# Kernel tuning notes

Measured on AMD Instinct MI355X. Metric: run time of the kernel, lower is better.

The kernel has to match this reference:

```python
import jax, jax.numpy as jnp
import numpy as np
from jax import lax

N = 4096
E = 131072
C = 128
CH = [(128, 256), (256, 512), (512, 512), (512, 256), (256, 128)]


def setup_inputs() -> dict:
    key = jax.random.key(0)
    ks = jax.random.split(key, 16)
    inp = {}
    inp["x"] = jax.random.normal(ks[0], (N, C), jnp.float32)
    src = jax.random.randint(ks[1], (E,), 0, N)
    dst = jax.random.randint(ks[2], (E,), 0, N)
    inp["edge_index"] = jnp.stack([src, dst]).astype(jnp.int32)
    for i, (ci, co) in enumerate(CH):
        inp[f"theta{i}"] = jax.random.normal(ks[3 + i], (ci, co), jnp.float32) / np.float32(np.sqrt(ci))
        inp[f"b{i}"] = jax.random.normal(ks[8 + i], (co,), jnp.float32) * 0.02
    inp["p1"] = jax.random.normal(ks[13], (256,), jnp.float32)
    inp["p2"] = jax.random.normal(ks[14], (512,), jnp.float32)
    return inp


def gcn(x, W, theta, b):
    """GCNConv with edge weights, dense-adjacency form.
    A_hat = W + I (self loops, weight 1); deg = row-sum of A_hat;
    out[i] = sum_{(r->i)} d^-1/2[r] * w * d^-1/2[i] * (x@theta)[r] + b."""
    n = W.shape[0]
    A = W + jnp.eye(n, dtype=W.dtype)
    deg = A.sum(axis=1)
    dinv = jnp.where(deg > 0, lax.rsqrt(deg), 0.0)
    An = dinv[:, None] * A * dinv[None, :]
    return An.T @ (x @ theta) + b


def augment_adj(W):
    """add_self_loops -> spspmm(A, A) -> remove_self_loops, dense form."""
    n = W.shape[0]
    A = W + jnp.eye(n, dtype=W.dtype)
    A2 = A @ A
    return A2 * (1.0 - jnp.eye(n, dtype=W.dtype))


def topk_pool(x, W, p, k):
    """TopKPooling (ratio fixed via static k, single graph)."""
    score = jnp.tanh((x @ p) / jnp.linalg.norm(p))
    vals, perm = lax.top_k(score, k)
    xp = x[perm] * vals[:, None]
    Wp = W[perm][:, perm]  # filter_adj on surviving nodes
    return xp, Wp, perm


def reference(x, edge_index, theta0, theta1, theta2, theta3, theta4,
              b0, b1, b2, b3, b4, p1, p2):
    n = x.shape[0]
    # dense weighted adjacency from edge list (edge_weight = ones, duplicates sum)
    W = jnp.zeros((n, n), x.dtype).at[edge_index[0], edge_index[1]].add(1.0)

    # down block 0
    x0 = jax.nn.relu(gcn(x, W, theta0, b0))                 # [N, 256]
    x1, W1, perm1 = topk_pool(x0, augment_adj(W), p1, n // 2)
    # down block 1
    x1b = jax.nn.relu(gcn(x1, W1, theta1, b1))              # [N/2, 512]
    x2, W2, perm2 = topk_pool(x1b, augment_adj(W1), p2, n // 4)
    # bottleneck block
    xb = jax.nn.relu(gcn(x2, W2, theta2, b2))               # [N/4, 512]
    summary = xb.mean(axis=0, keepdims=True)                # global_mean_pool, 1 graph
    # up block (i=3): edges[1]=W1, res=x1b, perm2
    up1 = jnp.zeros_like(x1b).at[perm2].set(xb)
    xu = jax.nn.relu(gcn(x1b + up1, W1, theta3, b3))        # [N/2, 256]
    # up block (i=4): edges[0]=W, res=x0, perm1
    up0 = jnp.zeros_like(x0).at[perm1].set(xu)
    xout = jax.nn.relu(gcn(x0 + up0, W, theta4, b4))        # [N, 128]
    return xout, summary
```

## Files before the change

kernel.cpp:

```cpp
#include <hip/hip_runtime.h>

#define N0 4096
#define P1K 2048
#define P2K 1024
#define SPLITS 4

typedef short bf16x8 __attribute__((ext_vector_type(8)));
typedef float f32x4 __attribute__((ext_vector_type(4)));

__device__ __forceinline__ unsigned short f2bf(float f) {
  unsigned int u = __float_as_uint(f);
  unsigned int r = (u + 0x7fff + ((u >> 16) & 1)) >> 16;
  return (unsigned short)r;
}
__device__ __forceinline__ float bf2f(unsigned short h) {
  unsigned int u = ((unsigned int)h) << 16;
  return __uint_as_float(u);
}

__device__ __forceinline__ float blockReduceSum256(float v) {
  __shared__ float sh[16];
  int lane = threadIdx.x & 63;
  int w = threadIdx.x >> 6;
#pragma unroll
// ... 66 lines not shown
    o0h[(size_t)n * 128 + k] = h;
    o0l[(size_t)n * 128 + k] = f2bf(v - bf2f(h));
  } else if (idx < 163840) {
    int i = idx - 32768;
    int k = i >> 9, n = i & 511;
    float v = t1[i];
    unsigned short h = f2bf(v);
    o1h[(size_t)n * 256 + k] = h;
    o1l[(size_t)n * 256 + k] = f2bf(v - bf2f(h));
  } else if (idx < 425984) {
    int i = idx - 163840;
    int k = i >> 9, n = i & 511;
    o2[(size_t)n * 512 + k] = f2bf(t2[i]);
  } else if (idx < 557056) {
    int i = idx - 425984;
    int k = i >> 8, n = i & 255;
    o3[(size_t)n * 512 + k] = f2bf(t3[i]);
  } else if (idx < 589824) {
    int i = idx - 557056;
    int k = i >> 7, n = i & 127;
    o4[(size_t)n * 256 + k] = f2bf(t4[i]);
  }
}

__global__ __launch_bounds__(256) void fused_ce_conv(
    const int* __restrict__ src, const int* __restrict__ dst, int* __restrict__ co,
    int* __restrict__ ci, int E, const float* t0, const float* t1, const float* t2,
    const float* t3, const float* t4, unsigned short* o0h, unsigned short* o0l,
    unsigned short* o1h, unsigned short* o1l, unsigned short* o2, unsigned short* o3,
    unsigned short* o4) {
  if (blockIdx.x < 512) count_edges_body(blockIdx.x, src, dst, co, ci, E);
  else conv_body(blockIdx.x - 512, t0, t1, t2, t3, t4, o0h, o0l, o1h, o1l, o2, o3, o4);
}

__global__ __launch_bounds__(1024) void exscan_dual(const int* __restrict__ co,
                                                    const int* __restrict__ ci,
                                                    int* __restrict__ optr,
                                                    int* __restrict__ iptr,
                                                    float* __restrict__ dinv0) {
  __shared__ int ls[1024];
  const int* cnt = blockIdx.x ? ci : co;
  int* ptr = blockIdx.x ? iptr : optr;
  int t = threadIdx.x;
  int v0 = cnt[t * 4], v1 = cnt[t * 4 + 1], v2 = cnt[t * 4 + 2], v3 = cnt[t * 4 + 3];
  int s = v0 + v1 + v2 + v3;
  ls[t] = s;
  __syncthreads();
  for (int off = 1; off < 1024; off <<= 1) {
    int x = (t >= off) ? ls[t - off] : 0;
    __syncthreads();
    ls[t] += x;
    __syncthreads();
  }
  int ex = (t > 0) ? ls[t - 1] : 0;
  ptr[t * 4]     = ex;
  ptr[t * 4 + 1] = ex + v0;
  ptr[t * 4 + 2] = ex + v0 + v1;
  ptr[t * 4 + 3] = ex + v0 + v1 + v2;
  if (t == 1023) ptr[4096] = ex + s;
  if (blockIdx.x == 0) {
    dinv0[t * 4]     = rsqrtf((float)v0 + 1.f);
    dinv0[t * 4 + 1] = rsqrtf((float)v1 + 1.f);
    dinv0[t * 4 + 2] = rsqrtf((float)v2 + 1.f);
    dinv0[t * 4 + 3] = rsqrtf((float)v3 + 1.f);
  }
}

__device__ __forceinline__ void fill_body(int b, const int* __restrict__ src,
                                          const int* __restrict__ dst,
                                          const int* __restrict__ optr,
                                          const int* __restrict__ iptr,
                                          int* __restrict__ fo, int* __restrict__ fi,
                                          int* __restrict__ odst, int* __restrict__ isrc,
                                          int E) {
  int e = b * 256 + threadIdx.x;
  if (e < E) {
    int s = src[e], d = dst[e];
    odst[optr[s] + atomicAdd(&fo[s], 1)] = d;
    isrc[iptr[d] + atomicAdd(&fi[d], 1)] = s;
  }
}

template <bool TOUT>
__device__ void gemm3_body(int bid, const float* __restrict__ A,
                           const unsigned short* __restrict__ BhT,
                           const unsigned short* __restrict__ BlT,
                           const int* __restrict__ permA, const float* __restrict__ valsA,
                           const float* __restrict__ dinv, float* __restrict__ C,
                           unsigned short* __restrict__ ChT, unsigned short* __restrict__ ClT,
                           int M, int N, int K, int nbx) {
  __shared__ unsigned short U[16384];
  unsigned short* Ah = U;
  unsigned short* Al = U + 4096;
  unsigned short* Bh = U + 8192;
  unsigned short* Bl = U + 12288;
  int tid = threadIdx.x;
  int by = bid / nbx, bx = bid % nbx;
  int row0 = by << 6, col0 = bx << 6;
  int l = tid & 63, wv = tid >> 6;
  int wr = (wv >> 1) << 5, wc = (wv & 1) << 5;
  f32x4 acc[2][2] = {};
  for (int k0 = 0; k0 < K; k0 += 64) {
#pragma unroll
    for (int it = 0; it < 2; ++it) {
      int idx = (it << 8) + tid;
      int r = idx >> 3, c8 = idx & 7;
      int sw = c8 ^ (r & 7);
      int row = row0 + r;
      int srow = permA ? permA[row] : row;
      float vs = valsA ? valsA[row] : 1.f;
      const float* Af = A + (size_t)srow * K + k0 + (c8 << 3);
      float4 f0 = *(const float4*)Af;
      float4 f1 = *(const float4*)(Af + 4);
      float vv[8] = {f0.x * vs, f0.y * vs, f0.z * vs, f0.w * vs,
                     f1.x * vs, f1.y * vs, f1.z * vs, f1.w * vs};
      uint4 uh, ul;
      unsigned short hh[8], ll[8];
#pragma unroll
      for (int q = 0; q < 8; ++q) {
        hh[q] = f2bf(vv[q]);
        ll[q] = f2bf(vv[q] - bf2f(hh[q]));
      }
      uh.x = (unsigned)hh[0] | ((unsigned)hh[1] << 16);
      uh.y = (unsigned)hh[2] | ((unsigned)hh[3] << 16);
      uh.z = (unsigned)hh[4] | ((unsigned)hh[5] << 16);
      uh.w = (unsigned)hh[6] | ((unsigned)hh[7] << 16);
      ul.x = (unsigned)ll[0] | ((unsigned)ll[1] << 16);
      ul.y = (unsigned)ll[2] | ((unsigned)ll[3] << 16);
      ul.z = (unsigned)ll[4] | ((unsigned)ll[5] << 16);
      ul.w = (unsigned)ll[6] | ((unsigned)ll[7] << 16);
      ((uint4*)Ah)[(r << 3) + sw] = uh;
      ((uint4*)Al)[(r << 3) + sw] = ul;
      ((uint4*)Bh)[(r << 3) + sw] =
          *(const uint4*)(BhT + (size_t)(col0 + r) * K + k0 + (c8 << 3));
      ((uint4*)Bl)[(r << 3) + sw] =
          *(const uint4*)(BlT + (size_t)(col0 + r) * K + k0 + (c8 << 3));
    }
    __syncthreads();
#pragma unroll
    for (int kk2 = 0; kk2 < 2; ++kk2) {
      int ch = (kk2 << 2) + (l >> 4);
      int ra = wr + (l & 15), rb = ra + 16;
      int ca = wc + (l & 15), cb = ca + 16;
      int oa0 = (ra << 6) + ((ch ^ (ra & 7)) << 3);
      int oa1 = (rb << 6) + ((ch ^ (rb & 7)) << 3);
      int ob0 = (ca << 6) + ((ch ^ (ca & 7)) << 3);
      int ob1 = (cb << 6) + ((ch ^ (cb & 7)) << 3);
      bf16x8 ah0 = *(const bf16x8*)&Ah[oa0], ah1 = *(const bf16x8*)&Ah[oa1];
      bf16x8 al0 = *(const bf16x8*)&Al[oa0], al1 = *(const bf16x8*)&Al[oa1];
      bf16x8 bh0 = *(const bf16x8*)&Bh[ob0], bh1 = *(const bf16x8*)&Bh[ob1];
      bf16x8 bl0 = *(const bf16x8*)&Bl[ob0], bl1 = *(const bf16x8*)&Bl[ob1];
      acc[0][0] = __builtin_amdgcn_mfma_f32_16x16x32_bf16(ah0, bh0, acc[0][0], 0, 0, 0);
      acc[0][1] = __builtin_amdgcn_mfma_f32_16x16x32_bf16(ah0, bh1, acc[0][1], 0, 0, 0);
      acc[1][0] = __builtin_amdgcn_mfma_f32_16x16x32_bf16(ah1, bh0, acc[1][0], 0, 0, 0);
      acc[1][1] = __builtin_amdgcn_mfma_f32_16x16x32_bf16(ah1, bh1, acc[1][1], 0, 0, 0);
      acc[0][0] = __builtin_amdgcn_mfma_f32_16x16x32_bf16(ah0, bl0, acc[0][0], 0, 0, 0);
      acc[0][1] = __builtin_amdgcn_mfma_f32_16x16x32_bf16(ah0, bl1, acc[0][1], 0, 0, 0);
      acc[1][0] = __builtin_amdgcn_mfma_f32_16x16x32_bf16(ah1, bl0, acc[1][0], 0, 0, 0);
      acc[1][1] = __builtin_amdgcn_mfma_f32_16x16x32_bf16(ah1, bl1, acc[1][1], 0, 0, 0);
      acc[0][0] = __builtin_amdgcn_mfma_f32_16x16x32_bf16(al0, bh0, acc[0][0], 0, 0, 0);
      acc[0][1] = __builtin_amdgcn_mfma_f32_16x16x32_bf16(al0, bh1, acc[0][1], 0, 0, 0);
      acc[1][0] = __builtin_amdgcn_mfma_f32_16x16x32_bf16(al1, bh0, acc[1][0], 0, 0, 0);
      acc[1][1] = __builtin_amdgcn_mfma_f32_16x16x32_bf16(al1, bh1, acc[1][1], 0, 0, 0);
    }
    __syncthreads();
  }
  int lrow = (l >> 4) << 2, lcol = l & 15;
  float* tf = (float*)U;
#pragma unroll
  for (int i = 0; i < 2; ++i)
#pragma unroll
    for (int j = 0; j < 2; ++j) {
      int lc = wc + (j << 4) + lcol;
      int lr0 = wr + (i << 4) + lrow;
      int c = col0 + lc;
#pragma unroll
      for (int rg = 0; rg < 4; ++rg) {
        int lr = lr0 + rg;
        int r = row0 + lr;
        float dv = dinv ? dinv[r] : 1.f;
        float v = acc[i][j][rg] * dv;
        C[(size_t)r * N + c] = v;
        if (TOUT) tf[lr * 65 + lc] = v;
      }
    }
  if (TOUT) {
    __syncthreads();
    for (int it = 0; it < 16; ++it) {
      int idx = (it << 8) + tid;
      int rr = idx >> 6, cc = idx & 63;
      float v = tf[cc * 65 + rr];
      unsigned short h = f2bf(v);
      size_t o = (size_t)(col0 + rr) * M + row0 + cc;
      ChT[o] = h;
      ClT[o] = f2bf(v - bf2f(h));
    }
  }
}

__global__ __launch_bounds__(256) void fused_fill_g3(
    const int* src, const int* dst, const int* optr, const int* iptr, int* fo, int* fi,
    int* odst, int* isrc, int E, const float* x, const unsigned short* t0hT,
    const unsigned short* t0lT, const float* dinv0, float* SA) {
  if (blockIdx.x < 512) fill_body(blockIdx.x, src, dst, optr, iptr, fo, fi, odst, isrc, E);
  else gemm3_body<false>(blockIdx.x - 512, x, t0hT, t0lT, nullptr, nullptr, dinv0, SA,
                         nullptr, nullptr, 4096, 256, 128, 4);
}

__device__ void transpose_body(int bid, const unsigned short* __restrict__ in,
                               unsigned short* __restrict__ out, int n) {
  __shared__ unsigned short t[64][65];
  int nb = n >> 6;
  int bx = bid % nb, by = bid / nb;
  int r0 = by << 6, c0 = bx << 6;
  for (int it = 0; it < 16; ++it) {
    int idx = (it << 8) + threadIdx.x;
    int r = idx >> 6, c = idx & 63;
    t[r][c] = in[(size_t)(r0 + r) * n + c0 + c];
  }
  __syncthreads();
  for (int it = 0; it < 16; ++it) {
    int idx = (it << 8) + threadIdx.x;
    int r = idx >> 6, c = idx & 63;
    out[(size_t)(c0 + r) * n + r0 + c] = t[c][r];
  }
}

__global__ __launch_bounds__(256) void fused_tr_g3(
    const unsigned short* W1b, unsigned short* W1bT, const float* x0,
    const unsigned short* t1hT, const unsigned short* t1lT, const int* perm1,
    const float* vals1, const float* dinv1, float* SA, unsigned short* ZhT,
    unsigned short* ZlT) {
  if (blockIdx.x < 1024) transpose_body(blockIdx.x, W1b, W1bT, 2048);
  else gemm3_body<true>(blockIdx.x - 1024, x0, t1hT, t1lT, perm1, vals1, dinv1, SA,
                        ZhT, ZlT, 2048, 512, 256, 8);
}

__global__ __launch_bounds__(256) void gemm_skd(const unsigned short* __restrict__ A,
                                                const unsigned short* __restrict__ BhT,
                                                const unsigned short* __restrict__ BlT,
                                                float* __restrict__ Pf,
                                                int M, int N, int K, int nbx, int nb2d) {
  __shared__ unsigned short As[4096], Bh[4096], Bl[4096];
  int tid = threadIdx.x;
  int s = blockIdx.x / nb2d;
  int r2 = blockIdx.x % nb2d;
  int by = r2 / nbx, bx = r2 % nbx;
  int row0 = by << 6, col0 = bx << 6;
  int kc = K / SPLITS;
  int ks = s * kc, ke = ks + kc;
  int l = tid & 63, wv = tid >> 6;
  int wr = (wv >> 1) << 5, wc = (wv & 1) << 5;
  f32x4 acc[2][2] = {};
  for (int k0 = ks; k0 < ke; k0 += 64) {
#pragma unroll
    for (int it = 0; it < 2; ++it) {
      int idx = (it << 8) + tid;
      int r = idx >> 3, c8 = idx & 7;
      int sw = c8 ^ (r & 7);
      ((uint4*)As)[(r << 3) + sw] =
          *(const uint4*)(A + (size_t)(row0 + r) * K + k0 + (c8 << 3));
      ((uint4*)Bh)[(r << 3) + sw] =
          *(const uint4*)(BhT + (size_t)(col0 + r) * K + k0 + (c8 << 3));
      ((uint4*)Bl)[(r << 3) + sw] =
          *(const uint4*)(BlT + (size_t)(col0 + r) * K + k0 + (c8 << 3));
    }
    __syncthreads();
#pragma unroll
    for (int kk2 = 0; kk2 < 2; ++kk2) {
      int ch = (kk2 << 2) + (l >> 4);
      int ra = wr + (l & 15), rb = ra + 16;
      int ca = wc + (l & 15), cb = ca + 16;
      bf16x8 a0 = *(const bf16x8*)&As[(ra << 6) + ((ch ^ (ra & 7)) << 3)];
      bf16x8 a1 = *(const bf16x8*)&As[(rb << 6) + ((ch ^ (rb & 7)) << 3)];
      bf16x8 bh0 = *(const bf16x8*)&Bh[(ca << 6) + ((ch ^ (ca & 7)) << 3)];
      bf16x8 bh1 = *(const bf16x8*)&Bh[(cb << 6) + ((ch ^ (cb & 7)) << 3)];
      bf16x8 bl0 = *(const bf16x8*)&Bl[(ca << 6) + ((ch ^ (ca & 7)) << 3)];
      bf16x8 bl1 = *(const bf16x8*)&Bl[(cb << 6) + ((ch ^ (cb & 7)) << 3)];
      acc[0][0] = __builtin_amdgcn_mfma_f32_16x16x32_bf16(a0, bh0, acc[0][0], 0, 0, 0);
      acc[0][1] = __builtin_amdgcn_mfma_f32_16x16x32_bf16(a0, bh1, acc[0][1], 0, 0, 0);
      acc[1][0] = __builtin_amdgcn_mfma_f32_16x16x32_bf16(a1, bh0, acc[1][0], 0, 0, 0);
      acc[1][1] = __builtin_amdgcn_mfma_f32_16x16x32_bf16(a1, bh1, acc[1][1], 0, 0, 0);
      acc[0][0] = __builtin_amdgcn_mfma_f32_16x16x32_bf16(a0, bl0, acc[0][0], 0, 0, 0);
      acc[0][1] = __builtin_amdgcn_mfma_f32_16x16x32_bf16(a0, bl1, acc[0][1], 0, 0, 0);
      acc[1][0] = __builtin_amdgcn_mfma_f32_16x16x32_bf16(a1, bl0, acc[1][0], 0, 0, 0);
      acc[1][1] = __builtin_amdgcn_mfma_f32_16x16x32_bf16(a1, bl1, acc[1][1], 0, 0, 0);
    }
    __syncthreads();
  }
  int lrow = (l >> 4) << 2, lcol = l & 15;
  float* P = Pf + (size_t)s * M * N;
#pragma unroll
  for (int i = 0; i < 2; ++i)
#pragma unroll
    for (int j = 0; j < 2; ++j) {
      int c = col0 + wc + (j << 4) + lcol;
      int r0 = row0 + wr + (i << 4) + lrow;
#pragma unroll
      for (int rg = 0; rg < 4; ++rg)
        P[(size_t)(r0 + rg) * N + c] = acc[i][j][rg];
    }
}

__global__ __launch_bounds__(256) void gemm_sk(const unsigned short* __restrict__ A,
                                               const unsigned short* __restrict__ BT,
                                               float* __restrict__ Pf,
                                               int M, int N, int K, int nbx, int nb2d) {
  __shared__ unsigned short As[4096];
  __shared__ unsigned short Bs[4096];
  int tid = threadIdx.x;
  int s = blockIdx.x / nb2d;
  int r2 = blockIdx.x % nb2d;
  int by = r2 / nbx, bx = r2 % nbx;
  int row0 = by << 6, col0 = bx << 6;
  int kc = K / SPLITS;
  int ks = s * kc, ke = ks + kc;
  int l = tid & 63, wv = tid >> 6;
  int wr = (wv >> 1) << 5, wc = (wv & 1) << 5;
  f32x4 acc[2][2] = {};
  for (int k0 = ks; k0 < ke; k0 += 64) {
#pragma unroll
    for (int it = 0; it < 2; ++it) {
      int idx = (it << 8) + tid;
      int r = idx >> 3, c8 = idx & 7;
      int sw = c8 ^ (r & 7);
      ((uint4*)As)[(r << 3) + sw] =
          *(const uint4*)(A + (size_t)(row0 + r) * K + k0 + (c8 << 3));
      ((uint4*)Bs)[(r << 3) + sw] =
          *(const uint4*)(BT + (size_t)(col0 + r) * K + k0 + (c8 << 3));
    }
    __syncthreads();
#pragma unroll
    for (int kk2 = 0; kk2 < 2; ++kk2) {
      int ch = (kk2 << 2) + (l >> 4);
      int ra = wr + (l & 15), rb = ra + 16;
      int ca = wc + (l & 15), cb = ca + 16;
      bf16x8 a0 = *(const bf16x8*)&As[(ra << 6) + ((ch ^ (ra & 7)) << 3)];
      bf16x8 a1 = *(const bf16x8*)&As[(rb << 6) + ((ch ^ (rb & 7)) << 3)];
      bf16x8 b0 = *(const bf16x8*)&Bs[(ca << 6) + ((ch ^ (ca & 7)) << 3)];
      bf16x8 b1 = *(const bf16x8*)&Bs[(cb << 6) + ((ch ^ (cb & 7)) << 3)];
      acc[0][0] = __builtin_amdgcn_mfma_f32_16x16x32_bf16(a0, b0, acc[0][0], 0, 0, 0);
      acc[0][1] = __builtin_amdgcn_mfma_f32_16x16x32_bf16(a0, b1, acc[0][1], 0, 0, 0);
      acc[1][0] = __builtin_amdgcn_mfma_f32_16x16x32_bf16(a1, b0, acc[1][0], 0, 0, 0);
      acc[1][1] = __builtin_amdgcn_mfma_f32_16x16x32_bf16(a1, b1, acc[1][1], 0, 0, 0);
    }
    __syncthreads();
  }
  int lrow = (l >> 4) << 2, lcol = l & 15;
  float* P = Pf + (size_t)s * M * N;
#pragma unroll
  for (int i = 0; i < 2; ++i)
#pragma unroll
    for (int j = 0; j < 2; ++j) {
      int c = col0 + wc + (j << 4) + lcol;
      int r0 = row0 + wr + (i << 4) + lrow;
#pragma unroll
      for (int rg = 0; rg < 4; ++rg)
        P[(size_t)(r0 + rg) * N + c] = acc[i][j][rg];
    }
}

__device__ void gemm_e_body(int bid, const float* __restrict__ A,
                            const unsigned short* __restrict__ BT,
                            const int* __restrict__ permA, const float* __restrict__ valsA,
                            const float* __restrict__ dinv, int dm,
                            float* __restrict__ Cf, unsigned short* __restrict__ CbT,
                            int M, int N, int K, int nbx) {
  __shared__ char gsm[16640];
  unsigned short* As = (unsigned short*)gsm;
  unsigned short* Bs = (unsigned short*)(gsm + 8192);
  int tid = threadIdx.x;
  int by = bid / nbx, bx = bid % nbx;
  int row0 = by << 6, col0 = bx << 6;
  int l = tid & 63, wv = tid >> 6;
  int wr = (wv >> 1) << 5, wc = (wv & 1) << 5;
  f32x4 acc[2][2] = {};
  for (int k0 = 0; k0 < K; k0 += 64) {
#pragma unroll
    for (int it = 0; it < 2; ++it) {
      int idx = (it << 8) + tid;
      int r = idx >> 3, c8 = idx & 7;
      int sw = c8 ^ (r & 7);
      int row = row0 + r;
      int srow = permA ? permA[row] : row;
      float vs = valsA ? valsA[row] : 1.f;
      const float* Af = A + (size_t)srow * K + k0 + (c8 << 3);
      float4 f0 = *(const float4*)Af;
      float4 f1 = *(const float4*)(Af + 4);
      uint4 u;
      u.x = (unsigned)f2bf(f0.x * vs) | ((unsigned)f2bf(f0.y * vs) << 16);
      u.y = (unsigned)f2bf(f0.z * vs) | ((unsigned)f2bf(f0.w * vs) << 16);
      u.z = (unsigned)f2bf(f1.x * vs) | ((unsigned)f2bf(f1.y * vs) << 16);
      u.w = (unsigned)f2bf(f1.z * vs) | ((unsigned)f2bf(f1.w * vs) << 16);
      ((uint4*)As)[(r << 3) + sw] = u;
      ((uint4*)Bs)[(r << 3) + sw] =
          *(const uint4*)(BT + (size_t)(col0 + r) * K + k0 + (c8 << 3));
    }
    __syncthreads();
#pragma unroll
    for (int kk2 = 0; kk2 < 2; ++kk2) {
      int ch = (kk2 << 2) + (l >> 4);
      int ra = wr + (l & 15), rb = ra + 16;
      int ca = wc + (l & 15), cb = ca + 16;
      bf16x8 a0 = *(const bf16x8*)&As[(ra << 6) + ((ch ^ (ra & 7)) << 3)];
      bf16x8 a1 = *(const bf16x8*)&As[(rb << 6) + ((ch ^ (rb & 7)) << 3)];
      bf16x8 b0 = *(const bf16x8*)&Bs[(ca << 6) + ((ch ^ (ca & 7)) << 3)];
      bf16x8 b1 = *(const bf16x8*)&Bs[(cb << 6) + ((ch ^ (cb & 7)) << 3)];
      acc[0][0] = __builtin_amdgcn_mfma_f32_16x16x32_bf16(a0, b0, acc[0][0], 0, 0, 0);
      acc[0][1] = __builtin_amdgcn_mfma_f32_16x16x32_bf16(a0, b1, acc[0][1], 0, 0, 0);
      acc[1][0] = __builtin_amdgcn_mfma_f32_16x16x32_bf16(a1, b0, acc[1][0], 0, 0, 0);
      acc[1][1] = __builtin_amdgcn_mfma_f32_16x16x32_bf16(a1, b1, acc[1][1], 0, 0, 0);
    }
    __syncthreads();
  }
  int lrow = (l >> 4) << 2, lcol = l & 15;
  float* tf = (float*)gsm;
#pragma unroll
  for (int i = 0; i < 2; ++i)
#pragma unroll
    for (int j = 0; j < 2; ++j) {
      int lc = wc + (j << 4) + lcol;
      int lr0 = wr + (i << 4) + lrow;
      int c = col0 + lc;
#pragma unroll
      for (int rg = 0; rg < 4; ++rg) {
        int lr = lr0 + rg;
        int r = row0 + lr;
        float dv = (dm == 1) ? dinv[r] : 1.f;
        float v = acc[i][j][rg] * dv;
        Cf[(size_t)r * N + c] = v;
        if (CbT) tf[lr * 65 + lc] = v;
      }
    }
  if (CbT) {
    __syncthreads();
    for (int it = 0; it < 16; ++it) {
      int idx = (it << 8) + tid;
      int rr = idx >> 6, cc = idx & 63;
      CbT[(size_t)(col0 + rr) * M + row0 + cc] = f2bf(tf[cc * 65 + rr]);
    }
  }
}

__global__ __launch_bounds__(256) void gemm_e_k(const float* A, const unsigned short* BT,
                                                const int* permA, const float* valsA,
                                                const float* dinv, int dm, float* Cf,
                                                unsigned short* CbT, int M, int N, int K,
                                                int nbx) {
  gemm_e_body(blockIdx.x, A, BT, permA, valsA, dinv, dm, Cf, CbT, M, N, K, nbx);
}

__device__ void mm_w2_body(int bid, const unsigned short* __restrict__ Wb,
                           const unsigned short* __restrict__ WbT,
                           const int* __restrict__ perm2, float* __restrict__ W2f,
                           float* __restrict__ degsum2) {
  __shared__ unsigned short As[4096];
  __shared__ unsigned short Bs[4096];
  __shared__ int pr[64], pc[64];
  int tid = threadIdx.x;
  int s = bid >> 8;
  int t2d = bid & 255;
  int bx = t2d & 15, by = t2d >> 4;
  int row0 = by << 6, col0 = bx << 6;
  int ks = s * 512, ke = ks + 512;
  if (tid < 64) pr[tid] = perm2[row0 + tid];
  else if (tid < 128) pc[tid - 64] = perm2[col0 + tid - 128 + 64];
  __syncthreads();
  int l = tid & 63, wv = tid >> 6;
  int wr = (wv >> 1) << 5, wc = (wv & 1) << 5;
  f32x4 acc[2][2] = {};
  for (int k0 = ks; k0 < ke; k0 += 64) {
#pragma unroll
    for (int it = 0; it < 2; ++it) {
      int idx = (it << 8) + tid;
      int r = idx >> 3, c8 = idx & 7;
      int sw = c8 ^ (r & 7);
      ((uint4*)As)[(r << 3) + sw] =
          *(const uint4*)(Wb + (size_t)pr[r] * 2048 + k0 + (c8 << 3));
      ((uint4*)Bs)[(r << 3) + sw] =
          *(const uint4*)(WbT + (size_t)pc[r] * 2048 + k0 + (c8 << 3));
    }
    __syncthreads();
    if (tid < 64) {
      int r = tid, d = pr[r] - k0;
      if (d >= 0 && d < 64) {
        int ui = (r << 6) + (((d >> 3) ^ (r & 7)) << 3) + (d & 7);
        As[ui] = f2bf(bf2f(As[ui]) + 1.f);
      }
    } else if (tid < 128) {
      int c = tid - 64, d = pc[c] - k0;
      if (d >= 0 && d < 64) {
        int ui = (c << 6) + (((d >> 3) ^ (c & 7)) << 3) + (d & 7);
        Bs[ui] = f2bf(bf2f(Bs[ui]) + 1.f);
      }
    }
    __syncthreads();
#pragma unroll
    for (int kk2 = 0; kk2 < 2; ++kk2) {
      int ch = (kk2 << 2) + (l >> 4);
      int ra = wr + (l & 15), rb = ra + 16;
      int ca = wc + (l & 15), cb = ca + 16;
      bf16x8 a0 = *(const bf16x8*)&As[(ra << 6) + ((ch ^ (ra & 7)) << 3)];
      bf16x8 a1 = *(const bf16x8*)&As[(rb << 6) + ((ch ^ (rb & 7)) << 3)];
      bf16x8 b0 = *(const bf16x8*)&Bs[(ca << 6) + ((ch ^ (ca & 7)) << 3)];
      bf16x8 b1 = *(const bf16x8*)&Bs[(cb << 6) + ((ch ^ (cb & 7)) << 3)];
      acc[0][0] = __builtin_amdgcn_mfma_f32_16x16x32_bf16(a0, b0, acc[0][0], 0, 0, 0);
      acc[0][1] = __builtin_amdgcn_mfma_f32_16x16x32_bf16(a0, b1, acc[0][1], 0, 0, 0);
      acc[1][0] = __builtin_amdgcn_mfma_f32_16x16x32_bf16(a1, b0, acc[1][0], 0, 0, 0);
      acc[1][1] = __builtin_amdgcn_mfma_f32_16x16x32_bf16(a1, b1, acc[1][1], 0, 0, 0);
    }
    __syncthreads();
  }
  int lrow = (l >> 4) << 2, lcol = l & 15;
#pragma unroll
  for (int i = 0; i < 2; ++i)
#pragma unroll
    for (int j = 0; j < 2; ++j) {
      int c = col0 + wc + (j << 4) + lcol;
      int r0 = row0 + wr + (i << 4) + lrow;
#pragma unroll
      for (int rg = 0; rg < 4; ++rg)
        atomicAdd(&W2f[(size_t)(r0 + rg) * 1024 + c], acc[i][j][rg]);
    }
#pragma unroll
  for (int i = 0; i < 2; ++i)
#pragma unroll
    for (int rg = 0; rg < 4; ++rg) {
      float rs = acc[i][0][rg] + acc[i][1][rg];
#pragma unroll
      for (int o = 1; o < 16; o <<= 1) rs += __shfl_xor(rs, o, 64);
      if ((l & 15) == 0) {
        int r = row0 + wr + (i << 4) + lrow + rg;
        atomicAdd(&degsum2[r], rs);
      }
    }
}

__global__ __launch_bounds__(256) void fused_w2_g2a(
    const unsigned short* Wb, const unsigned short* WbT, const int* perm2, float* W2f,
    float* degsum2, const float* x1b, const unsigned short* t2T, const float* vals2,
    float* SA, unsigned short* SAbT) {
  if (blockIdx.x < 1024) mm_w2_body(blockIdx.x, Wb, WbT, perm2, W2f, degsum2);
  else gemm_e_body(blockIdx.x - 1024, x1b, t2T, perm2, vals2, nullptr, 0, SA, SAbT,
                   1024, 512, 512, 8);
}

__global__ __launch_bounds__(256) void w2T(const float* __restrict__ W2f,
                                           const float* __restrict__ degsum2,
                                           unsigned short* __restrict__ W2Tb,
                                           float* __restrict__ dinv2v) {
  __shared__ float t[64][65];
  __shared__ float ds[64];
  int bx = blockIdx.x & 15, by = blockIdx.x >> 4;
  int r0 = by << 6, c0 = bx << 6;
  if (threadIdx.x < 64) {
    int r = r0 + threadIdx.x;
    float dg = degsum2[r] - W2f[(size_t)r * 1024 + r];
    float dv = rsqrtf(dg + 1.f);
    ds[threadIdx.x] = dv;
    if (bx == 0) dinv2v[r] = dv;
  }
  for (int it = 0; it < 16; ++it) {
    int idx = (it << 8) + threadIdx.x;
    int r = idx >> 6, c = idx & 63;
    float v = W2f[(size_t)(r0 + r) * 1024 + c0 + c];
    if (r0 + r == c0 + c) v = 0.f;
    t[r][c] = v;
  }
  __syncthreads();
  for (int it = 0; it < 16; ++it) {
    int idx = (it << 8) + threadIdx.x;
    int rr = idx >> 6, cc = idx & 63;
    W2Tb[(size_t)(c0 + rr) * 1024 + r0 + cc] = f2bf(t[cc][rr] * ds[cc]);
  }
}

__global__ __launch_bounds__(256) void epi_red1(const float* __restrict__ Pf,
                                                const float* __restrict__ Zadd,
                                                const float* __restrict__ dinv,
                                                const float* __restrict__ bias,
                                                const int* __restrict__ permS,
                                                float* __restrict__ scatterDst,
                                                float* __restrict__ outp, int M, int N,
                                                int zs) {
  int g = blockIdx.x * 256 + threadIdx.x;
  size_t base = (size_t)g * 4;
  size_t MN = (size_t)M * N;
  if (base >= MN) return;
  int r = (int)(base / N), c = (int)(base % N);
  float4 a = *(const float4*)&Pf[base];
#pragma unroll
  for (int s = 1; s < SPLITS; ++s) {
    float4 p = *(const float4*)&Pf[s * MN + base];
    a.x += p.x; a.y += p.y; a.z += p.z; a.w += p.w;
  }
  float4 z = *(const float4*)&Zadd[base];
  float dv = dinv[r];
  float zf = zs ? dv : 1.f;
  float4 bb = *(const float4*)&bias[c];
  float4 o;
  o.x = fmaxf(dv * (a.x + zf * z.x) + bb.x, 0.f);
  o.y = fmaxf(dv * (a.y + zf * z.y) + bb.y, 0.f);
  o.z = fmaxf(dv * (a.z + zf * z.z) + bb.z, 0.f);
  o.w = fmaxf(dv * (a.w + zf * z.w) + bb.w, 0.f);
  if (outp) *(float4*)&outp[base] = o;
  if (permS) {
    float4* d = (float4*)&scatterDst[(size_t)permS[r] * N + c];
    float4 cur = *d;
    cur.x += o.x; cur.y += o.y; cur.z += o.z; cur.w += o.w;
    *d = cur;
  }
}

__global__ __launch_bounds__(256) void epi_red1s(const float* __restrict__ Pf,
                                                 const float* __restrict__ Zadd,
                                                 const float* __restrict__ dinv,
                                                 const float* __restrict__ bias,
                                                 const float* __restrict__ pvec,
                                                 float* __restrict__ sc,
                                                 float* __restrict__ outp) {
  __shared__ float shs[2][2][2];
  int li = threadIdx.x & 127;
  int lr = threadIdx.x >> 7;
  int r = blockIdx.x * 2 + lr;
  size_t base = (size_t)r * 512 + li * 4;
  const size_t MN = (size_t)2048 * 512;
  float4 a = *(const float4*)&Pf[base];
#pragma unroll
  for (int s = 1; s < SPLITS; ++s) {
    float4 p = *(const float4*)&Pf[s * MN + base];
    a.x += p.x; a.y += p.y; a.z += p.z; a.w += p.w;
  }
  float4 z = *(const float4*)&Zadd[base];
  float dv = dinv[r];
  float4 bb = *(const float4*)&bias[li * 4];
  float4 o;
  o.x = fmaxf(dv * (a.x + z.x) + bb.x, 0.f);
  o.y = fmaxf(dv * (a.y + z.y) + bb.y, 0.f);
  o.z = fmaxf(dv * (a.z + z.z) + bb.z, 0.f);
  o.w = fmaxf(dv * (a.w + z.w) + bb.w, 0.f);
  *(float4*)&outp[base] = o;
  float4 pv = *(const float4*)&pvec[li * 4];
  float s1 = pv.x * pv.x + pv.y * pv.y + pv.z * pv.z + pv.w * pv.w;
  float s2 = o.x * pv.x + o.y * pv.y + o.z * pv.z + o.w * pv.w;
#pragma unroll
  for (int t = 32; t > 0; t >>= 1) {
    s1 += __shfl_down(s1, t, 64);
    s2 += __shfl_down(s2, t, 64);
  }
  int wir = (threadIdx.x >> 6) & 1;
  if ((threadIdx.x & 63) == 0) { shs[lr][wir][0] = s1; shs[lr][wir][1] = s2; }
  __syncthreads();
  if ((threadIdx.x & 127) == 0) {
    float S1 = shs[lr][0][0] + shs[lr][1][0];
    float S2 = shs[lr][0][1] + shs[lr][1][1];
    sc[r] = tanhf(S2 / sqrtf(S1));
  }
}

template <int C, bool SCORE>
__global__ __launch_bounds__(256) void gcn_spmm4(const int* __restrict__ iptr,
                                                 const int* __restrict__ isrc,
                                                 const float* __restrict__ Z,
                                                 const float* __restrict__ dinv,
                                                 const float* __restrict__ bias,
                                                 const float* __restrict__ pvec,
                                                 float* __restrict__ sc,
                                                 float* __restrict__ outp) {
  constexpr int L = C / 4;
  int li = threadIdx.x % L;
  int i = blockIdx.x * (256 / L) + threadIdx.x / L;
  float4 acc = *(const float4*)(Z + (size_t)i * C + li * 4);
  int beg = iptr[i], end = iptr[i + 1];
  for (int e = beg; e < end; ++e) {
    float4 z = *(const float4*)(Z + (size_t)isrc[e] * C + li * 4);
    acc.x += z.x; acc.y += z.y; acc.z += z.z; acc.w += z.w;
  }
  float d = dinv[i];
  float4 bb = *(const float4*)(bias + li * 4);
  float4 o;
  o.x = fmaxf(d * acc.x + bb.x, 0.f);
  o.y = fmaxf(d * acc.y + bb.y, 0.f);
  o.z = fmaxf(d * acc.z + bb.z, 0.f);
  o.w = fmaxf(d * acc.w + bb.w, 0.f);
  *(float4*)(outp + (size_t)i * C + li * 4) = o;
  if (SCORE) {
    float4 pv = *(const float4*)(pvec + li * 4);
    float s1 = pv.x * pv.x + pv.y * pv.y + pv.z * pv.z + pv.w * pv.w;
    float s2 = o.x * pv.x + o.y * pv.y + o.z * pv.z + o.w * pv.w;
#pragma unroll
    for (int t = 32; t > 0; t >>= 1) {
      s1 += __shfl_down(s1, t, 64);
      s2 += __shfl_down(s2, t, 64);
    }
    if ((threadIdx.x & 63) == 0) sc[i] = tanhf(s2 / sqrtf(s1));
  }
}

__global__ __launch_bounds__(1024) void topk_select(const float* __restrict__ score,
                                                    int n, int k, int* __restrict__ perm,
                                                    float* __restrict__ vals,
                                                    int* __restrict__ rank) {
  __shared__ unsigned int keys[4096];
  __shared__ int hist[256];
  __shared__ int wsums[16];
  __shared__ unsigned int sh_prefix;
  __shared__ int sh_rem;
  int t = threadIdx.x;
  int m = n >> 10;
  for (int i = t; i < n; i += 1024) {
    unsigned int u = __float_as_uint(score[i]);
    keys[i] = u ^ ((unsigned int)((int)u >> 31) | 0x80000000u);
  }
  if (t == 0) { sh_prefix = 0u; sh_rem = k; }
  __syncthreads();
  for (int round = 0; round < 4; ++round) {
    int shift = 24 - (round << 3);
    if (t < 256) hist[t] = 0;
    __syncthreads();
    unsigned int prefix = sh_prefix;
    unsigned int maskhi = (round == 0) ? 0u : (0xFFFFFFFFu << (shift + 8));
    for (int i = t; i < n; i += 1024) {
      unsigned int kk = keys[i];
      if ((kk & maskhi) == prefix) atomicAdd(&hist[(kk >> shift) & 255], 1);
    }
    __syncthreads();
    if (t == 0) {
      int rem = sh_rem, acc = 0, b = 255;
      for (; b > 0; --b) {
        if (acc + hist[b] >= rem) break;
        acc += hist[b];
      }
      sh_rem = rem - acc;
      sh_prefix = prefix | ((unsigned int)b << shift);
    }
    __syncthreads();
  }
  unsigned int thr = sh_prefix;
  int need = sh_rem;
  int base = t * m;
  int f[4];
  int cnt = 0;
#pragma unroll
  for (int j = 0; j < 4; ++j) {
    f[j] = 0;
    if (j < m) { f[j] = (keys[base + j] == thr) ? 1 : 0; cnt += f[j]; }
  }
  int ex = blockScanExclusive(cnt, wsums);
  int sel[4];
  int scnt = 0;
#pragma unroll
  for (int j = 0; j < 4; ++j) {
    sel[j] = 0;
    if (j < m) {
      unsigned int kk = keys[base + j];
      sel[j] = (kk > thr) || (kk == thr && ex < need);
      ex += f[j];
      scnt += sel[j];
    }
  }
  int pos = blockScanExclusive(scnt, wsums);
#pragma unroll
  for (int j = 0; j < 4; ++j) {
    if (j < m) {
      int i = base + j;
      if (sel[j]) {
        unsigned int kk = keys[i];
        unsigned int u = (kk & 0x80000000u) ? (kk ^ 0x80000000u) : ~kk;
        perm[pos] = i;
        vals[pos] = __uint_as_float(u);
        rank[i] = pos;
        pos++;
      } else {
        rank[i] = -1;
      }
    }
  }
}

__global__ __launch_bounds__(256) void build_W1(const int* __restrict__ optr,
                                                const int* __restrict__ odst,
                                                const int* __restrict__ perm1,
                                                const int* __restrict__ rank1,
                                                unsigned short* __restrict__ W1b,
                                                float* __restrict__ dinv1) {
  __shared__ float row[2048];
  int a = blockIdx.x;
  int pa = perm1[a];
  for (int i = threadIdx.x; i < 2048; i += 256) row[i] = 0.f;
  __syncthreads();
  int kbeg = optr[pa], kend = optr[pa + 1];
  int nk = kend - kbeg + 1;
  int wv = threadIdx.x >> 6, lane = threadIdx.x & 63;
  for (int kidx = wv; kidx < nk; kidx += 4) {
    int k = (kidx == 0) ? pa : odst[kbeg + kidx - 1];
    int jbeg = optr[k], jend = optr[k + 1];
    for (int jj = jbeg - 1 + lane; jj < jend; jj += 64) {
      int j = (jj < jbeg) ? k : odst[jj];
      int rb = rank1[j];
      if (rb >= 0) atomicAdd(&row[rb], 1.0f);
    }
  }
  __syncthreads();
  float ssum = 0.f;
  for (int i = threadIdx.x; i < 2048; i += 256) {
    float v = (i == a) ? 0.f : row[i];
    W1b[(size_t)a * 2048 + i] = f2bf(v);
    ssum += v;
  }
  float t = blockReduceSum256(ssum);
  if (threadIdx.x == 0) dinv1[a] = rsqrtf(t + 1.0f);
}

__device__ void mean_cols_body(int c, const float* __restrict__ X, int R, int C,
                               float* __restrict__ outp) {
  float s = 0.f;
  for (int r = threadIdx.x; r < R; r += 256) s += X[(size_t)r * C + c];
  float t = blockReduceSum256(s);
  if (threadIdx.x == 0) outp[c] = t / (float)R;
}

__global__ __launch_bounds__(256) void fused_mean_up1a(
    const float* xb, float* meanOut, const float* x1b, const unsigned short* t3T,
    const float* dinv1, float* SA, unsigned short* SAbT) {
  if (blockIdx.x < 512) mean_cols_body(blockIdx.x, xb, 1024, 512, meanOut);
  else gemm_e_body(blockIdx.x - 512, x1b, t3T, nullptr, nullptr, dinv1, 1, SA, SAbT,
                   2048, 256, 512, 4);
}

extern "C" void kernel_launch(void* const* d_in, const int* in_sizes, int n_in,
                              void* d_out, int out_size, void* d_ws, size_t ws_size,
                              hipStream_t stream) {
  const float* x      = (const float*)d_in[0];
  const int*   eidx   = (const int*)d_in[1];
  const float* theta0 = (const float*)d_in[2];
  const float* b0     = (const float*)d_in[3];
  const float* theta1 = (const float*)d_in[4];
  const float* b1     = (const float*)d_in[5];
  const float* theta2 = (const float*)d_in[6];
  const float* b2     = (const float*)d_in[7];
  const float* theta3 = (const float*)d_in[8];
  const float* b3     = (const float*)d_in[9];
  const float* theta4 = (const float*)d_in[10];
  const float* b4     = (const float*)d_in[11];
  const float* p1     = (const float*)d_in[12];
  const float* p2     = (const float*)d_in[13];
  const int E = in_sizes[1] / 2;
  const int* src = eidx;
  const int* dst = eidx + E;
  float* out = (float*)d_out;

  char* wsb = (char*)d_ws;
  size_t off = 0;
  auto alloc = [&](size_t bytes) -> void* {
    void* p = wsb + off;
    off = (off + bytes + 255) & ~(size_t)255;
    return p;
  };
  char* zblock = (char*)alloc((size_t)4 * N0 * 4 + P2K * 4 + (size_t)P2K * P2K * 4);
  int* cnt4 = (int*)zblock;
  float* degsum2 = (float*)(zblock + (size_t)4 * N0 * 4);
  float* W2f = (float*)(zblock + (size_t)4 * N0 * 4 + P2K * 4);
  size_t zbytes = (size_t)4 * N0 * 4 + P2K * 4 + (size_t)P2K * P2K * 4;

  int* optr  = (int*)alloc((N0 + 1) * 4);
  int* iptr  = (int*)alloc((N0 + 1) * 4);
  int* odst  = (int*)alloc((size_t)E * 4);
  int* isrc  = (int*)alloc((size_t)E * 4);
  int* perm1 = (int*)alloc(P1K * 4);
  int* rank1 = (int*)alloc(N0 * 4);
  int* perm2 = (int*)alloc(P2K * 4);
  int* rank2 = (int*)alloc(P1K * 4);
  float* dinv0 = (float*)alloc(N0 * 4);
  float* dinv1 = (float*)alloc(P1K * 4);
  float* dinv2v = (float*)alloc(P2K * 4);
  float* vals1 = (float*)alloc(P1K * 4);
  float* vals2 = (float*)alloc(P2K * 4);
  float* score = (float*)alloc(N0 * 4);
  float* x0  = (float*)alloc((size_t)N0 * 256 * 4);
  float* x1b = (float*)alloc((size_t)P1K * 512 * 4);
  float* xb  = (float*)alloc((size_t)P2K * 512 * 4);
  float* SA  = (float*)alloc((size_t)P1K * 512 * 4);
  float* Pf  = (float*)alloc((size_t)SPLITS * 1048576 * 4);
  unsigned short* W1b  = (unsigned short*)alloc((size_t)P1K * P1K * 2);
  unsigned short* W1bT = (unsigned short*)alloc((size_t)P1K * P1K * 2);
  unsigned short* W2Tb = (unsigned short*)alloc((size_t)P2K * P2K * 2);
  unsigned short* SAbT = (unsigned short*)alloc((size_t)524288 * 2);
  unsigned short* ZhT  = (unsigned short*)alloc((size_t)512 * 2048 * 2);
  unsigned short* ZlT  = (unsigned short*)alloc((size_t)512 * 2048 * 2);
  unsigned short* t0hT = (unsigned short*)alloc((size_t)256 * 128 * 2);
  unsigned short* t0lT = (unsigned short*)alloc((size_t)256 * 128 * 2);
  unsigned short* t1hT = (unsigned short*)alloc((size_t)512 * 256 * 2);
  unsigned short* t1lT = (unsigned short*)alloc((size_t)512 * 256 * 2);
  unsigned short* t2T  = (unsigned short*)alloc((size_t)512 * 512 * 2);
  unsigned short* t3T  = (unsigned short*)alloc((size_t)256 * 512 * 2);
  unsigned short* t4T  = (unsigned short*)alloc((size_t)128 * 256 * 2);
  (void)ws_size; (void)n_in; (void)out_size;

  int* co = cnt4;
  int* ci = cnt4 + N0;
  int* fo = cnt4 + 2 * N0;
  int* fi = cnt4 + 3 * N0;

  hipMemsetAsync(zblock, 0, zbytes, stream);
  fused_ce_conv<<<512 + 2304, 256, 0, stream>>>(src, dst, co, ci, E, theta0, theta1,
                                                theta2, theta3, theta4, t0hT, t0lT,
                                                t1hT, t1lT, t2T, t3T, t4T);
  exscan_dual<<<2, 1024, 0, stream>>>(co, ci, optr, iptr, dinv0);
  fused_fill_g3<<<512 + 256, 256, 0, stream>>>(src, dst, optr, iptr, fo, fi, odst, isrc,
                                               E, x, t0hT, t0lT, dinv0, SA);
  gcn_spmm4<256, true><<<1024, 256, 0, stream>>>(iptr, isrc, SA, dinv0, b0, p1, score, x0);

  topk_select<<<1, 1024, 0, stream>>>(score, 4096, 2048, perm1, vals1, rank1);
  build_W1<<<2048, 256, 0, stream>>>(optr, odst, perm1, rank1, W1b, dinv1);
  fused_tr_g3<<<1024 + 256, 256, 0, stream>>>(W1b, W1bT, x0, t1hT, t1lT, perm1, vals1,
                                              dinv1, SA, ZhT, ZlT);

  gemm_skd<<<256 * SPLITS, 256, 0, stream>>>(W1bT, ZhT, ZlT, Pf, 2048, 512, 2048, 8, 256);
  epi_red1s<<<1024, 256, 0, stream>>>(Pf, SA, dinv1, b1, p2, score, x1b);

  topk_select<<<1, 1024, 0, stream>>>(score, 2048, 1024, perm2, vals2, rank2);
  fused_w2_g2a<<<1024 + 128, 256, 0, stream>>>(W1b, W1bT, perm2, W2f, degsum2, x1b, t2T,
                                               vals2, SA, SAbT);
  w2T<<<256, 256, 0, stream>>>(W2f, degsum2, W2Tb, dinv2v);

  gemm_sk<<<128 * SPLITS, 256, 0, stream>>>(W2Tb, SAbT, Pf, 1024, 512, 1024, 8, 128);
  epi_red1<<<1024 * 512 / 1024, 256, 0, stream>>>(Pf, SA, dinv2v, b2, perm2, x1b, xb,
                                                  1024, 512, 1);
  fused_mean_up1a<<<512 + 128, 256, 0, stream>>>(xb, out + 524288, x1b, t3T, dinv1,
                                                 SA, SAbT);

  gemm_sk<<<128 * SPLITS, 256, 0, stream>>>(W1bT, SAbT, Pf, 2048, 256, 2048, 4, 128);
  epi_red1<<<2048 * 256 / 1024, 256, 0, stream>>>(Pf, SA, dinv1, b3, perm1, x0, nullptr,
                                                  2048, 256, 0);

  gemm_e_k<<<128, 256, 0, stream>>>(x0, t4T, nullptr, nullptr, dinv0, 1, SA, nullptr,
                                    4096, 128, 256, 2);
  gcn_spmm4<128, false><<<512, 256, 0, stream>>>(iptr, isrc, SA, dinv0, b4, nullptr,
                                                 nullptr, out);
}
```

Baseline: 310.1 us.

## Fold self-loop term into adjacency diagonal and share LDS across fused branches

The self-loop contribution is now encoded by writing 1 on the diagonal of the bf16 W1/W2 adjacency matrices. Previously it was added separately in the epilogues from an fp32 SA buffer. This removes the SA writes in the feature GEMMs and the Zadd reads in the reduction epilogues, and drops the per-tile diagonal patch in mm_w2. Shared memory in the fused kernels is now one buffer sized for the larger branch instead of separate static arrays, which lowers LDS per block. The risk is that the self-loop term now passes through bf16 operands, and the A² computation depends on the diagonal being exactly 1.

```diff
diff --git a/kernel.cpp b/kernel.cpp
--- a/kernel.cpp
+++ b/kernel.cpp
@@ -172,14 +172,14 @@
 }
 
 template <bool TOUT>
-__device__ void gemm3_body(int bid, const float* __restrict__ A,
+__device__ void gemm3_body(char* smem, int bid, const float* __restrict__ A,
                            const unsigned short* __restrict__ BhT,
                            const unsigned short* __restrict__ BlT,
                            const int* __restrict__ permA, const float* __restrict__ valsA,
                            const float* __restrict__ dinv, float* __restrict__ C,
                            unsigned short* __restrict__ ChT, unsigned short* __restrict__ ClT,
                            int M, int N, int K, int nbx) {
-  __shared__ unsigned short U[16384];
+  unsigned short* U = (unsigned short*)smem;
   unsigned short* Ah = U;
   unsigned short* Al = U + 4096;
   unsigned short* Bh = U + 8192;
@@ -256,7 +256,7 @@
     __syncthreads();
   }
   int lrow = (l >> 4) << 2, lcol = l & 15;
-  float* tf = (float*)U;
+  float* tf = (float*)smem;
 #pragma unroll
   for (int i = 0; i < 2; ++i)
 #pragma unroll
@@ -270,7 +270,7 @@
         int r = row0 + lr;
         float dv = dinv ? dinv[r] : 1.f;
         float v = acc[i][j][rg] * dv;
-        C[(size_t)r * N + c] = v;
+        if (C) C[(size_t)r * N + c] = v;
         if (TOUT) tf[lr * 65 + lc] = v;
       }
     }
@@ -292,38 +292,39 @@
     const int* src, const int* dst, const int* optr, const int* iptr, int* fo, int* fi,
     int* odst, int* isrc, int E, const float* x, const unsigned short* t0hT,
     const unsigned short* t0lT, const float* dinv0, float* SA) {
+  __shared__ char smem[32768];
   if (blockIdx.x < 512) fill_body(blockIdx.x, src, dst, optr, iptr, fo, fi, odst, isrc, E);
-  else gemm3_body<false>(blockIdx.x - 512, x, t0hT, t0lT, nullptr, nullptr, dinv0, SA,
-                         nullptr, nullptr, 4096, 256, 128, 4);
-}
-
-__device__ void transpose_body(int bid, const unsigned short* __restrict__ in,
+  else gemm3_body<false>(smem, blockIdx.x - 512, x, t0hT, t0lT, nullptr, nullptr, dinv0,
+                         SA, nullptr, nullptr, 4096, 256, 128, 4);
+}
+
+__device__ void transpose_body(char* smem, int bid, const unsigned short* __restrict__ in,
                                unsigned short* __restrict__ out, int n) {
-  __shared__ unsigned short t[64][65];
+  unsigned short* t = (unsigned short*)smem;
   int nb = n >> 6;
   int bx = bid % nb, by = bid / nb;
   int r0 = by << 6, c0 = bx << 6;
   for (int it = 0; it < 16; ++it) {
     int idx = (it << 8) + threadIdx.x;
     int r = idx >> 6, c = idx & 63;
-    t[r][c] = in[(size_t)(r0 + r) * n + c0 + c];
+    t[r * 65 + c] = in[(size_t)(r0 + r) * n + c0 + c];
   }
   __syncthreads();
   for (int it = 0; it < 16; ++it) {
     int idx = (it << 8) + threadIdx.x;
     int r = idx >> 6, c = idx & 63;
-    out[(size_t)(c0 + r) * n + r0 + c] = t[c][r];
+    out[(size_t)(c0 + r) * n + r0 + c] = t[c * 65 + r];
   }
 }
 
 __global__ __launch_bounds__(256) void fused_tr_g3(
     const unsigned short* W1b, unsigned short* W1bT, const float* x0,
     const unsigned short* t1hT, const unsigned short* t1lT, const int* perm1,
-    const float* vals1, const float* dinv1, float* SA, unsigned short* ZhT,
-    unsigned short* ZlT) {
-  if (blockIdx.x < 1024) transpose_body(blockIdx.x, W1b, W1bT, 2048);
-  else gemm3_body<true>(blockIdx.x - 1024, x0, t1hT, t1lT, perm1, vals1, dinv1, SA,
-                        ZhT, ZlT, 2048, 512, 256, 8);
+    const float* vals1, const float* dinv1, unsigned short* ZhT, unsigned short* ZlT) {
+  __shared__ char smem[32768];
+  if (blockIdx.x < 1024) transpose_body(smem, blockIdx.x, W1b, W1bT, 2048);
+  else gemm3_body<true>(smem, blockIdx.x - 1024, x0, t1hT, t1lT, perm1, vals1, dinv1,
+                        nullptr, ZhT, ZlT, 2048, 512, 256, 8);
 }
 
 __global__ __launch_bounds__(256) void gemm_skd(const unsigned short* __restrict__ A,
@@ -450,15 +451,14 @@
     }
 }
 
-__device__ void gemm_e_body(int bid, const float* __restrict__ A,
+__device__ void gemm_e_body(char* smem, int bid, const float* __restrict__ A,
                             const unsigned short* __restrict__ BT,
                             const int* __restrict__ permA, const float* __restrict__ valsA,
                             const float* __restrict__ dinv, int dm,
                             float* __restrict__ Cf, unsigned short* __restrict__ CbT,
                             int M, int N, int K, int nbx) {
-  __shared__ char gsm[16640];
-  unsigned short* As = (unsigned short*)gsm;
-  unsigned short* Bs = (unsigned short*)(gsm + 8192);
+  unsigned short* As = (unsigned short*)smem;
+  unsigned short* Bs = (unsigned short*)(smem + 8192);
   int tid = threadIdx.x;
   int by = bid / nbx, bx = bid % nbx;
   int row0 = by << 6, col0 = bx << 6;
@@ -504,7 +504,7 @@
     __syncthreads();
   }
   int lrow = (l >> 4) << 2, lcol = l & 15;
-  float* tf = (float*)gsm;
+  float* tf = (float*)smem;
 #pragma unroll
   for (int i = 0; i < 2; ++i)
 #pragma unroll
@@ -518,7 +518,7 @@
         int r = row0 + lr;
         float dv = (dm == 1) ? dinv[r] : 1.f;
         float v = acc[i][j][rg] * dv;
-        Cf[(size_t)r * N + c] = v;
+        if (Cf) Cf[(size_t)r * N + c] = v;
         if (CbT) tf[lr * 65 + lc] = v;
       }
     }
@@ -537,16 +537,18 @@
                                                 const float* dinv, int dm, float* Cf,
                                                 unsigned short* CbT, int M, int N, int K,
                                                 int nbx) {
-  gemm_e_body(blockIdx.x, A, BT, permA, valsA, dinv, dm, Cf, CbT, M, N, K, nbx);
-}
-
-__device__ void mm_w2_body(int bid, const unsigned short* __restrict__ Wb,
+  __shared__ char smem[16640];
+  gemm_e_body(smem, blockIdx.x, A, BT, permA, valsA, dinv, dm, Cf, CbT, M, N, K, nbx);
+}
+
+__device__ void mm_w2_body(char* smem, int bid, const unsigned short* __restrict__ Wb,
                            const unsigned short* __restrict__ WbT,
                            const int* __restrict__ perm2, float* __restrict__ W2f,
                            float* __restrict__ degsum2) {
-  __shared__ unsigned short As[4096];
-  __shared__ unsigned short Bs[4096];
-  __shared__ int pr[64], pc[64];
+  unsigned short* As = (unsigned short*)smem;
+  unsigned short* Bs = (unsigned short*)(smem + 8192);
+  int* pr = (int*)(smem + 16384);
+  int* pc = pr + 64;
   int tid = threadIdx.x;
   int s = bid >> 8;
   int t2d = bid & 255;
@@ -569,20 +571,6 @@
           *(const uint4*)(Wb + (size_t)pr[r] * 2048 + k0 + (c8 << 3));
       ((uint4*)Bs)[(r << 3) + sw] =
           *(const uint4*)(WbT + (size_t)pc[r] * 2048 + k0 + (c8 << 3));
-    }
-    __syncthreads();
-    if (tid < 64) {
-      int r = tid, d = pr[r] - k0;
-      if (d >= 0 && d < 64) {
-        int ui = (r << 6) + (((d >> 3) ^ (r & 7)) << 3) + (d & 7);
-        As[ui] = f2bf(bf2f(As[ui]) + 1.f);
-      }
-    } else if (tid < 128) {
-      int c = tid - 64, d = pc[c] - k0;
-      if (d >= 0 && d < 64) {
-        int ui = (c << 6) + (((d >> 3) ^ (c & 7)) << 3) + (d & 7);
-        Bs[ui] = f2bf(bf2f(Bs[ui]) + 1.f);
-      }
     }
     __syncthreads();
 #pragma unroll
@@ -629,10 +617,11 @@
 __global__ __launch_bounds__(256) void fused_w2_g2a(
     const unsigned short* Wb, const unsigned short* WbT, const int* perm2, float* W2f,
     float* degsum2, const float* x1b, const unsigned short* t2T, const float* vals2,
-    float* SA, unsigned short* SAbT) {
-  if (blockIdx.x < 1024) mm_w2_body(blockIdx.x, Wb, WbT, perm2, W2f, degsum2);
-  else gemm_e_body(blockIdx.x - 1024, x1b, t2T, perm2, vals2, nullptr, 0, SA, SAbT,
-                   1024, 512, 512, 8);
+    unsigned short* SAbT) {
+  __shared__ char smem[16896];
+  if (blockIdx.x < 1024) mm_w2_body(smem, blockIdx.x, Wb, WbT, perm2, W2f, degsum2);
+  else gemm_e_body(smem, blockIdx.x - 1024, x1b, t2T, perm2, vals2, nullptr, 0,
+                   nullptr, SAbT, 1024, 512, 512, 8);
 }
 
 __global__ __launch_bounds__(256) void w2T(const float* __restrict__ W2f,
@@ -654,7 +643,7 @@
     int idx = (it << 8) + threadIdx.x;
     int r = idx >> 6, c = idx & 63;
     float v = W2f[(size_t)(r0 + r) * 1024 + c0 + c];
-    if (r0 + r == c0 + c) v = 0.f;
+    if (r0 + r == c0 + c) v = 1.f;
     t[r][c] = v;
   }
   __syncthreads();
@@ -666,13 +655,11 @@
 }
 
 __global__ __launch_bounds__(256) void epi_red1(const float* __restrict__ Pf,
-                                                const float* __restrict__ Zadd,
                                                 const float* __restrict__ dinv,
                                                 const float* __restrict__ bias,
                                                 const int* __restrict__ permS,
                                                 float* __restrict__ scatterDst,
-                                                float* __restrict__ outp, int M, int N,
-                                                int zs) {
+                                                float* __restrict__ outp, int M, int N) {
   int g = blockIdx.x * 256 + threadIdx.x;
   size_t base = (size_t)g * 4;
   size_t MN = (size_t)M * N;
@@ -684,15 +671,13 @@
     float4 p = *(const float4*)&Pf[s * MN + base];
     a.x += p.x; a.y += p.y; a.z += p.z; a.w += p.w;
   }
-  float4 z = *(const float4*)&Zadd[base];
   float dv = dinv[r];
-  float zf = zs ? dv : 1.f;
   float4 bb = *(const float4*)&bias[c];
   float4 o;
-  o.x = fmaxf(dv * (a.x + zf * z.x) + bb.x, 0.f);
-  o.y = fmaxf(dv * (a.y + zf * z.y) + bb.y, 0.f);
-  o.z = fmaxf(dv * (a.z + zf * z.z) + bb.z, 0.f);
-  o.w = fmaxf(dv * (a.w + zf * z.w) + bb.w, 0.f);
+  o.x = fmaxf(dv * a.x + bb.x, 0.f);
+  o.y = fmaxf(dv * a.y + bb.y, 0.f);
+  o.z = fmaxf(dv * a.z + bb.z, 0.f);
+  o.w = fmaxf(dv * a.w + bb.w, 0.f);
   if (outp) *(float4*)&outp[base] = o;
   if (permS) {
     float4* d = (float4*)&scatterDst[(size_t)permS[r] * N + c];
@@ -703,7 +688,6 @@
 }
 
 __global__ __launch_bounds__(256) void epi_red1s(const float* __restrict__ Pf,
-                                                 const float* __restrict__ Zadd,
                                                  const float* __restrict__ dinv,
                                                  const float* __restrict__ bias,
                                                  const float* __restrict__ pvec,
@@ -721,14 +705,13 @@
     float4 p = *(const float4*)&Pf[s * MN + base];
     a.x += p.x; a.y += p.y; a.z += p.z; a.w += p.w;
   }
-  float4 z = *(const float4*)&Zadd[base];
   float dv = dinv[r];
   float4 bb = *(const float4*)&bias[li * 4];
   float4 o;
-  o.x = fmaxf(dv * (a.x + z.x) + bb.x, 0.f);
-  o.y = fmaxf(dv * (a.y + z.y) + bb.y, 0.f);
-  o.z = fmaxf(dv * (a.z + z.z) + bb.z, 0.f);
-  o.w = fmaxf(dv * (a.w + z.w) + bb.w, 0.f);
+  o.x = fmaxf(dv * a.x + bb.x, 0.f);
+  o.y = fmaxf(dv * a.y + bb.y, 0.f);
+  o.z = fmaxf(dv * a.z + bb.z, 0.f);
+  o.w = fmaxf(dv * a.w + bb.w, 0.f);
   *(float4*)&outp[base] = o;
   float4 pv = *(const float4*)&pvec[li * 4];
   float s1 = pv.x * pv.x + pv.y * pv.y + pv.z * pv.z + pv.w * pv.w;
@@ -894,9 +877,9 @@
   __syncthreads();
   float ssum = 0.f;
   for (int i = threadIdx.x; i < 2048; i += 256) {
-    float v = (i == a) ? 0.f : row[i];
-    W1b[(size_t)a * 2048 + i] = f2bf(v);
-    ssum += v;
+    float v = row[i];
+    W1b[(size_t)a * 2048 + i] = f2bf((i == a) ? 1.f : v);
+    ssum += (i == a) ? 0.f : v;
   }
   float t = blockReduceSum256(ssum);
   if (threadIdx.x == 0) dinv1[a] = rsqrtf(t + 1.0f);
@@ -912,10 +895,11 @@
 
 __global__ __launch_bounds__(256) void fused_mean_up1a(
     const float* xb, float* meanOut, const float* x1b, const unsigned short* t3T,
-    const float* dinv1, float* SA, unsigned short* SAbT) {
+    const float* dinv1, unsigned short* SAbT) {
+  __shared__ char smem[16640];
   if (blockIdx.x < 512) mean_cols_body(blockIdx.x, xb, 1024, 512, meanOut);
-  else gemm_e_body(blockIdx.x - 512, x1b, t3T, nullptr, nullptr, dinv1, 1, SA, SAbT,
-                   2048, 256, 512, 4);
+  else gemm_e_body(smem, blockIdx.x - 512, x1b, t3T, nullptr, nullptr, dinv1, 1,
+                   nullptr, SAbT, 2048, 256, 512, 4);
 }
 
 extern "C" void kernel_launch(void* const* d_in, const int* in_sizes, int n_in,
@@ -1004,25 +988,24 @@
   topk_select<<<1, 1024, 0, stream>>>(score, 4096, 2048, perm1, vals1, rank1);
   build_W1<<<2048, 256, 0, stream>>>(optr, odst, perm1, rank1, W1b, dinv1);
   fused_tr_g3<<<1024 + 256, 256, 0, stream>>>(W1b, W1bT, x0, t1hT, t1lT, perm1, vals1,
-                                              dinv1, SA, ZhT, ZlT);
+                                              dinv1, ZhT, ZlT);
 
   gemm_skd<<<256 * SPLITS, 256, 0, stream>>>(W1bT, ZhT, ZlT, Pf, 2048, 512, 2048, 8, 256);
-  epi_red1s<<<1024, 256, 0, stream>>>(Pf, SA, dinv1, b1, p2, score, x1b);
+  epi_red1s<<<1024, 256, 0, stream>>>(Pf, dinv1, b1, p2, score, x1b);
 
   topk_select<<<1, 1024, 0, stream>>>(score, 2048, 1024, perm2, vals2, rank2);
   fused_w2_g2a<<<1024 + 128, 256, 0, stream>>>(W1b, W1bT, perm2, W2f, degsum2, x1b, t2T,
-                                               vals2, SA, SAbT);
+                                               vals2, SAbT);
   w2T<<<256, 256, 0, stream>>>(W2f, degsum2, W2Tb, dinv2v);
 
   gemm_sk<<<128 * SPLITS, 256, 0, stream>>>(W2Tb, SAbT, Pf, 1024, 512, 1024, 8, 128);
-  epi_red1<<<1024 * 512 / 1024, 256, 0, stream>>>(Pf, SA, dinv2v, b2, perm2, x1b, xb,
-                                                  1024, 512, 1);
-  fused_mean_up1a<<<512 + 128, 256, 0, stream>>>(xb, out + 524288, x1b, t3T, dinv1,
-                                                 SA, SAbT);
+  epi_red1<<<1024 * 512 / 1024, 256, 0, stream>>>(Pf, dinv2v, b2, perm2, x1b, xb,
+                                                  1024, 512);
+  fused_mean_up1a<<<512 + 128, 256, 0, stream>>>(xb, out + 524288, x1b, t3T, dinv1, SAbT);
 
   gemm_sk<<<128 * SPLITS, 256, 0, stream>>>(W1bT, SAbT, Pf, 2048, 256, 2048, 4, 128);
-  epi_red1<<<2048 * 256 / 1024, 256, 0, stream>>>(Pf, SA, dinv1, b3, perm1, x0, nullptr,
-                                                  2048, 256, 0);
+  epi_red1<<<2048 * 256 / 1024, 256, 0, stream>>>(Pf, dinv1, b3, perm1, x0, nullptr,
+                                                  2048, 256);
 
   gemm_e_k<<<128, 256, 0, stream>>>(x0, t4T, nullptr, nullptr, dinv0, 1, SA, nullptr,
                                     4096, 128, 256, 2);
```

Result: faster. 302.3 us, median of 2 (-2.5%).
